# Kernel tuning notes

Measured on AMD Instinct MI355X. Metric: run time of the kernel, lower is better.

The kernel has to match this reference:

```python
import jax, jax.numpy as jnp
import numpy as np

FEATURE_DIM = 512
ACTION_DIM = 32
N_EXPERTS = 4
D_HIDDEN = 256
BATCH = 131072


def setup_inputs() -> dict:
    key = jax.random.key(0)
    ks = jax.random.split(key, 7)
    s_in = 1.0 / np.sqrt(FEATURE_DIM)
    s_h = 1.0 / np.sqrt(D_HIDDEN)
    return {
        "features": jax.random.normal(ks[0], (BATCH, FEATURE_DIM), dtype=jnp.float32),
        # gating network: feature_dim -> n_experts
        "Wg": jax.random.normal(ks[1], (FEATURE_DIM, N_EXPERTS), dtype=jnp.float32) * s_in,
        "bg": jnp.zeros((N_EXPERTS,), dtype=jnp.float32),
        # per-expert 2-layer MLP: feature_dim -> d_hidden -> action_dim
        "W1": jax.random.normal(ks[2], (N_EXPERTS, FEATURE_DIM, D_HIDDEN), dtype=jnp.float32) * s_in,
        "b1": jnp.zeros((N_EXPERTS, D_HIDDEN), dtype=jnp.float32),
        "W2": jax.random.normal(ks[3], (N_EXPERTS, D_HIDDEN, ACTION_DIM), dtype=jnp.float32) * s_h,
        "b2": jnp.zeros((N_EXPERTS, ACTION_DIM), dtype=jnp.float32),
    }


def reference(features, Wg, bg, W1, b1, W2, b2):
    # gate: softmax over experts, shape [b, e]
    gate = jax.nn.softmax(features @ Wg + bg, axis=-1)
    # expert MLPs (dense MoE: every expert sees every token)
    h = jax.nn.relu(jnp.einsum("bf,efh->beh", features, W1) + b1)  # [b, e, h]
    expert_out = jnp.einsum("beh,eha->bea", h, W2) + b2            # [b, e, a]
    # gate-weighted mixture -> action mean [b, a]
    action_mean = jnp.einsum("bea,be->ba", expert_out, gate)
    return action_mean
```

## Files before the change

kernel.cpp:

```cpp
#include <hip/hip_runtime.h>
#include <hip/hip_bf16.h>
#include <math.h>

#define FDIM 512
#define NEXP 4
#define HDIM 256
#define ADIM 32
#define BM   128
#define NTHR 512

typedef __attribute__((ext_vector_type(8))) short frag8;
typedef __attribute__((ext_vector_type(4))) float f32x4;

#define W1T_OFF 0
#define W2T_OFF (4*256*512)
#define WGT_OFF (W2T_OFF + 4*32*256)

__device__ inline ushort f2bf(float x) {
    union { float f; unsigned u; } v; v.f = x;
    unsigned r = v.u + 0x7FFFu + ((v.u >> 16) & 1u);
    return (ushort)(r >> 16);
}

__device__ inline frag8 pack8(f32x4 a, f32x4 b) {
    frag8 r;
    r[0] = (short)f2bf(a[0]); r[1] = (short)f2bf(a[1]);
    r[2] = (short)f2bf(a[2]); r[3] = (short)f2bf(a[3]);
    r[4] = (short)f2bf(b[0]); r[5] = (short)f2bf(b[1]);
    r[6] = (short)f2bf(b[2]); r[7] = (short)f2bf(b[3]);
    return r;
}

__device__ __forceinline__ void gl16(const void* g, void* l) {
    __builtin_amdgcn_global_load_lds(
        (const __attribute__((address_space(1))) unsigned int*)g,
        (__attribute__((address_space(3))) unsigned int*)l, 16, 0, 0);
}

__global__ __launch_bounds__(256) void moe_prep(const float* __restrict__ Wg,
                                                const float* __restrict__ W1,
                                                const float* __restrict__ W2,
                                                ushort* __restrict__ ws) {
    const int b = blockIdx.x, t = threadIdx.x;
    if (b < 64) {
        #pragma unroll
        for (int it = 0; it < 4; ++it) {
            int oct = (b * 256 + t) + it * 16384;
            int n = oct & 255, k8 = (oct >> 8) & 63, e = oct >> 14;
            f32x4 v0, v1;
            #pragma unroll
            for (int j = 0; j < 4; ++j) v0[j] = W1[(e*512 + k8*8 + j)*256 + n];
            #pragma unroll
            for (int j = 0; j < 4; ++j) v1[j] = W1[(e*512 + k8*8 + 4 + j)*256 + n];
            *(frag8*)(ws + W1T_OFF + (e*HDIM + n)*FDIM + k8*8) = pack8(v0, v1);
        }
    } else if (b < 80) {
        int oct = (b - 64) * 256 + t;
        int a = oct & 31, n8 = (oct >> 5) & 31, e = oct >> 10;
        f32x4 v0, v1;
        #pragma unroll
        for (int j = 0; j < 4; ++j) v0[j] = W2[(e*HDIM + n8*8 + j)*ADIM + a];
        #pragma unroll
        for (int j = 0; j < 4; ++j) v1[j] = W2[(e*HDIM + n8*8 + 4 + j)*ADIM + a];
        *(frag8*)(ws + W2T_OFF + (e*ADIM + a)*HDIM + n8*8) = pack8(v0, v1);
    } else {
        int oct = (b - 80) * 256 + t;
        int k8 = oct & 63, c = oct >> 6;
        f32x4 v0 = {0,0,0,0}, v1 = {0,0,0,0};
        if (c < NEXP) {
            #pragma unroll
            for (int j = 0; j < 4; ++j) v0[j] = Wg[(k8*8 + j)*NEXP + c];
            #pragma unroll
            for (int j = 0; j < 4; ++j) v1[j] = Wg[(k8*8 + 4 + j)*NEXP + c];
        }
        *(frag8*)(ws + WGT_OFF + c*FDIM + k8*8) = pack8(v0, v1);
    }
}

__global__ __launch_bounds__(NTHR, 2) void moe_main(
        const float* __restrict__ feat, const float* __restrict__ bg,
        const float* __restrict__ b1,  const float* __restrict__ b2,
        const ushort* __restrict__ ws, float* __restrict__ out) {
    __shared__ __attribute__((aligned(16))) unsigned char smem[65536 + 65536 + 16384 + 2048];
    unsigned char* bufA = smem;
    unsigned char* bufB = smem + 65536;
    unsigned char* wgtb = smem + 131072;
    float*         wgate = (float*)(smem + 147456);

    const int tid = threadIdx.x;
    const int lane = tid & 63;
    const int wave = tid >> 6;
    const int l15 = lane & 15;
    const int lg  = lane >> 4;
    const int row0 = blockIdx.x * BM;
    const int wrow = row0 + wave * 16;
    const ushort* w2t = ws + W2T_OFF;
    const char* w1b = (const char*)(ws + W1T_OFF);
    const char* wgb = (const char*)(ws + WGT_OFF);

    int sOff[8];
    #pragma unroll
    for (int j = 0; j < 8; ++j) {
        int slot = j * 512 + tid;
        int col  = slot >> 4;
        int kkp  = ((slot & 15) * 16) ^ ((col & 7) << 4);
        sOff[j]  = col * 1024 + kkp;
    }
    int gOff[2];
    #pragma unroll
    for (int j = 0; j < 2; ++j) {
        int slot = j * 512 + tid;
        int col  = slot >> 6;
        int off  = (slot & 63) * 16;
        gOff[j]  = col * 1024 + (off ^ ((col & 7) << 4));
    }

    #pragma unroll
    for (int j = 0; j < 2; ++j)
        gl16(wgb + gOff[j], wgtb + j * 8192 + wave * 1024);
    #pragma unroll
    for (int j = 0; j < 8; ++j)
        gl16(w1b + sOff[j], bufA + j * 8192 + wave * 1024);

    frag8 afrag[16];
    const float* fp = feat + (size_t)(wrow + l15) * FDIM + lg * 8;
    #pragma unroll
    for (int g4 = 0; g4 < 4; ++g4) {
        f32x4 t0[4], t1[4];
        #pragma unroll
        for (int s = 0; s < 4; ++s) {
            const float* p = fp + (g4 * 4 + s) * 32;
            t0[s] = *(const f32x4*)p;
            t1[s] = *(const f32x4*)(p + 4);
        }
        #pragma unroll
        for (int s = 0; s < 4; ++s) afrag[g4 * 4 + s] = pack8(t0[s], t1[s]);
    }

    __syncthreads();

    {
        f32x4 ga = {0.f, 0.f, 0.f, 0.f};
        #pragma unroll
        for (int s = 0; s < 16; ++s) {
            frag8 bb = *(const frag8*)(wgtb + l15 * 1024 + ((s * 64 + lg * 16) ^ ((l15 & 7) << 4)));
            ga = __builtin_amdgcn_mfma_f32_16x16x32_bf16(afrag[s], bb, ga, 0, 0, 0);
        }
        float bgv = bg[l15 & 3];
        #pragma unroll
        for (int r = 0; r < 4; ++r) {
            float v = ga[r] + bgv;
            float m = fmaxf(v, __shfl_xor(v, 1));
            m = fmaxf(m, __shfl_xor(m, 2));
            float eV = expf(v - m);
            float sV = eV + __shfl_xor(eV, 1);
            sV += __shfl_xor(sV, 2);
            float g = eV / sV;
            if (l15 < NEXP) wgate[wave * 64 + (lg * 4 + r) * 4 + l15] = g;
        }
    }

    f32x4 act[2];
    act[0] = (f32x4){0.f, 0.f, 0.f, 0.f};
    act[1] = (f32x4){0.f, 0.f, 0.f, 0.f};

    for (int e = 0; e < NEXP; ++e) {
        f32x4 acc1[16];
        #pragma unroll
        for (int ct = 0; ct < 16; ++ct) acc1[ct] = (f32x4){0.f, 0.f, 0.f, 0.f};

        const char* wbase = w1b + e * 262144;

        #pragma unroll
        for (int c = 0; c < 4; ++c) {
            if (c < 3) {
                unsigned char* dst = ((c + 1) & 1) ? bufB : bufA;
                #pragma unroll
                for (int j = 0; j < 8; ++j)
                    gl16(wbase + (c + 1) * 256 + sOff[j], dst + j * 8192 + wave * 1024);
            }
            __syncthreads();
            unsigned char* src = (c & 1) ? bufB : bufA;
            #pragma unroll
            for (int s = 0; s < 4; ++s) {
                #pragma unroll
                for (int ct = 0; ct < 16; ++ct) {
                    frag8 bb = *(const frag8*)(src + (ct * 16 + l15) * 256 +
                                               ((s * 64 + lg * 16) ^ ((l15 & 7) << 4)));
                    acc1[ct] = __builtin_amdgcn_mfma_f32_16x16x32_bf16(
                        afrag[c * 4 + s], bb, acc1[ct], 0, 0, 0);
                }
            }
            if (c < 3) __syncthreads();
        }

        unsigned char* hb = bufA + wave * 8192;
        #pragma unroll
        for (int ct = 0; ct < 16; ++ct) {
            float b1v = b1[e * HDIM + ct * 16 + l15];
            #pragma unroll
            for (int r = 0; r < 4; ++r) {
                int row = lg * 4 + r;
                float v = fmaxf(acc1[ct][r] + b1v, 0.f);
                *(ushort*)(hb + row * 512 + (((ct * 16 + l15) * 2) ^ ((row & 7) << 4))) = f2bf(v);
            }
        }
        asm volatile("s_waitcnt lgkmcnt(0)" ::: "memory");
        __builtin_amdgcn_sched_barrier(0);

        f32x4 acc2[2];
        acc2[0] = (f32x4){0.f, 0.f, 0.f, 0.f};
        acc2[1] = (f32x4){0.f, 0.f, 0.f, 0.f};
        #pragma unroll
        for (int s2 = 0; s2 < 8; ++s2) {
            frag8 ha = *(const frag8*)(hb + l15 * 512 + ((s2 * 64 + lg * 16) ^ ((l15 & 7) << 4)));
            #pragma unroll
            for (int ct2 = 0; ct2 < 2; ++ct2) {
                frag8 bb = *(const frag8*)(w2t + (e * ADIM + ct2 * 16 + l15) * HDIM + (s2 * 4 + lg) * 8);
                acc2[ct2] = __builtin_amdgcn_mfma_f32_16x16x32_bf16(ha, bb, acc2[ct2], 0, 0, 0);
            }
        }
        #pragma unroll
        for (int ct2 = 0; ct2 < 2; ++ct2) {
            float b2v = b2[e * ADIM + ct2 * 16 + l15];
            #pragma unroll
            for (int r = 0; r < 4; ++r) {
                float g = wgate[wave * 64 + (lg * 4 + r) * 4 + e];
                act[ct2][r] += g * (acc2[ct2][r] + b2v);
            }
        }

        if (e < 3) {
            __syncthreads();
            const char* nb = w1b + (e + 1) * 262144;
            #pragma unroll
            for (int j = 0; j < 8; ++j)
                gl16(nb + sOff[j], bufA + j * 8192 + wave * 1024);
        }
    }

    #pragma unroll
    for (int ct2 = 0; ct2 < 2; ++ct2)
        #pragma unroll
        for (int r = 0; r < 4; ++r)
            out[(size_t)(wrow + lg * 4 + r) * ADIM + ct2 * 16 + l15] = act[ct2][r];
}

extern "C" void kernel_launch(void* const* d_in, const int* in_sizes, int n_in,
                              void* d_out, int out_size, void* d_ws, size_t ws_size,
                              hipStream_t stream) {
    const float* feat = (const float*)d_in[0];
    const float* Wg   = (const float*)d_in[1];
    const float* bg   = (const float*)d_in[2];
    const float* W1   = (const float*)d_in[3];
    const float* b1   = (const float*)d_in[4];
    const float* W2   = (const float*)d_in[5];
    const float* b2   = (const float*)d_in[6];
    float* out = (float*)d_out;
    ushort* ws = (ushort*)d_ws;

    moe_prep<<<84, 256, 0, stream>>>(Wg, W1, W2, ws);
    const int nblk = 131072 / BM;
    moe_main<<<nblk, NTHR, 0, stream>>>(feat, bg, b1, b2, ws, out);
}
```

Before: 694.6 us.

## Split hidden dim into halves with continuous double-buffered W1 pipeline across experts

Each expert's layer-1 GEMM is split into two 128-column halves, and the 32KB W1 chunks are streamed through a ping-pong buffer as one continuous 32-step pipeline across experts and halves. This removes the per-expert pipeline drain and reload stall. W2 is now staged into LDS instead of being read from global memory inside the layer-2 loop, and the hidden activations get a dedicated LDS region. The change halves the acc1 register footprint, which frees VGPRs, but it adds a barrier on every chunk and depends on the buffer-ordering logic across iterations being correct.

```diff
diff --git a/kernel.cpp b/kernel.cpp
--- a/kernel.cpp
+++ b/kernel.cpp
@@ -81,10 +81,11 @@
         const float* __restrict__ feat, const float* __restrict__ bg,
         const float* __restrict__ b1,  const float* __restrict__ b2,
         const ushort* __restrict__ ws, float* __restrict__ out) {
-    __shared__ __attribute__((aligned(16))) unsigned char smem[65536 + 65536 + 16384 + 2048];
-    unsigned char* bufA = smem;
-    unsigned char* bufB = smem + 65536;
-    unsigned char* wgtb = smem + 131072;
+    __shared__ __attribute__((aligned(16))) unsigned char smem[149504];
+    unsigned char* buf0 = smem;
+    unsigned char* buf1 = smem + 32768;
+    unsigned char* w2b  = smem + 65536;
+    unsigned char* hbuf = smem + 81920;
     float*         wgate = (float*)(smem + 147456);
 
     const int tid = threadIdx.x;
@@ -94,47 +95,44 @@
     const int lg  = lane >> 4;
     const int row0 = blockIdx.x * BM;
     const int wrow = row0 + wave * 16;
-    const ushort* w2t = ws + W2T_OFF;
     const char* w1b = (const char*)(ws + W1T_OFF);
+    const char* w2g = (const char*)(ws + W2T_OFF);
     const char* wgb = (const char*)(ws + WGT_OFF);
 
-    int sOff[8];
-    #pragma unroll
-    for (int j = 0; j < 8; ++j) {
-        int slot = j * 512 + tid;
-        int col  = slot >> 4;
-        int kkp  = ((slot & 15) * 16) ^ ((col & 7) << 4);
-        sOff[j]  = col * 1024 + kkp;
-    }
-    int gOff[2];
+    int thrOff[4], w2Off[2], gOff[2];
+    #pragma unroll
+    for (int j = 0; j < 4; ++j) {
+        int slot = j * 512 + tid, cl = slot >> 4;
+        thrOff[j] = cl * 1024 + (((slot & 15) * 16) ^ ((cl & 7) << 4));
+    }
     #pragma unroll
     for (int j = 0; j < 2; ++j) {
-        int slot = j * 512 + tid;
-        int col  = slot >> 6;
-        int off  = (slot & 63) * 16;
-        gOff[j]  = col * 1024 + (off ^ ((col & 7) << 4));
-    }
-
-    #pragma unroll
-    for (int j = 0; j < 2; ++j)
-        gl16(wgb + gOff[j], wgtb + j * 8192 + wave * 1024);
-    #pragma unroll
-    for (int j = 0; j < 8; ++j)
-        gl16(w1b + sOff[j], bufA + j * 8192 + wave * 1024);
+        int slot = j * 512 + tid, c2 = slot >> 5;
+        w2Off[j] = c2 * 512 + (((slot & 31) * 16) ^ ((c2 & 7) << 4));
+        int cg = slot >> 6;
+        gOff[j] = cg * 1024 + (((slot & 63) * 16) ^ ((cg & 7) << 4));
+    }
+
+    #pragma unroll
+    for (int j = 0; j < 2; ++j) gl16(wgb + gOff[j], buf1 + j * 8192 + wave * 1024);
+    #pragma unroll
+    for (int j = 0; j < 4; ++j) gl16(w1b + thrOff[j], buf0 + j * 8192 + wave * 1024);
 
     frag8 afrag[16];
-    const float* fp = feat + (size_t)(wrow + l15) * FDIM + lg * 8;
-    #pragma unroll
-    for (int g4 = 0; g4 < 4; ++g4) {
-        f32x4 t0[4], t1[4];
-        #pragma unroll
-        for (int s = 0; s < 4; ++s) {
-            const float* p = fp + (g4 * 4 + s) * 32;
-            t0[s] = *(const f32x4*)p;
-            t1[s] = *(const f32x4*)(p + 4);
-        }
-        #pragma unroll
-        for (int s = 0; s < 4; ++s) afrag[g4 * 4 + s] = pack8(t0[s], t1[s]);
+    {
+        const float* fp = feat + (size_t)(wrow + l15) * FDIM + lg * 8;
+        #pragma unroll
+        for (int g4 = 0; g4 < 4; ++g4) {
+            f32x4 t0[4], t1[4];
+            #pragma unroll
+            for (int s = 0; s < 4; ++s) {
+                const float* p = fp + (g4 * 4 + s) * 32;
+                t0[s] = *(const f32x4*)p;
+                t1[s] = *(const f32x4*)(p + 4);
+            }
+            #pragma unroll
+            for (int s = 0; s < 4; ++s) afrag[g4 * 4 + s] = pack8(t0[s], t1[s]);
+        }
     }
 
     __syncthreads();
@@ -143,7 +141,7 @@
         f32x4 ga = {0.f, 0.f, 0.f, 0.f};
         #pragma unroll
         for (int s = 0; s < 16; ++s) {
-            frag8 bb = *(const frag8*)(wgtb + l15 * 1024 + ((s * 64 + lg * 16) ^ ((l15 & 7) << 4)));
+            frag8 bb = *(const frag8*)(buf1 + l15 * 1024 + ((s * 64 + lg * 16) ^ ((l15 & 7) << 4)));
             ga = __builtin_amdgcn_mfma_f32_16x16x32_bf16(afrag[s], bb, ga, 0, 0, 0);
         }
         float bgv = bg[l15 & 3];
@@ -155,87 +153,94 @@
             float eV = expf(v - m);
             float sV = eV + __shfl_xor(eV, 1);
             sV += __shfl_xor(sV, 2);
-            float g = eV / sV;
-            if (l15 < NEXP) wgate[wave * 64 + (lg * 4 + r) * 4 + l15] = g;
-        }
-    }
+            if (l15 < NEXP) wgate[wave * 64 + (lg * 4 + r) * 4 + l15] = eV / sV;
+        }
+    }
+    __syncthreads();
 
     f32x4 act[2];
     act[0] = (f32x4){0.f, 0.f, 0.f, 0.f};
     act[1] = (f32x4){0.f, 0.f, 0.f, 0.f};
 
     for (int e = 0; e < NEXP; ++e) {
-        f32x4 acc1[16];
-        #pragma unroll
-        for (int ct = 0; ct < 16; ++ct) acc1[ct] = (f32x4){0.f, 0.f, 0.f, 0.f};
-
-        const char* wbase = w1b + e * 262144;
-
-        #pragma unroll
-        for (int c = 0; c < 4; ++c) {
-            if (c < 3) {
-                unsigned char* dst = ((c + 1) & 1) ? bufB : bufA;
-                #pragma unroll
-                for (int j = 0; j < 8; ++j)
-                    gl16(wbase + (c + 1) * 256 + sOff[j], dst + j * 8192 + wave * 1024);
-            }
-            __syncthreads();
-            unsigned char* src = (c & 1) ? bufB : bufA;
-            #pragma unroll
-            for (int s = 0; s < 4; ++s) {
-                #pragma unroll
-                for (int ct = 0; ct < 16; ++ct) {
-                    frag8 bb = *(const frag8*)(src + (ct * 16 + l15) * 256 +
-                                               ((s * 64 + lg * 16) ^ ((l15 & 7) << 4)));
-                    acc1[ct] = __builtin_amdgcn_mfma_f32_16x16x32_bf16(
-                        afrag[c * 4 + s], bb, acc1[ct], 0, 0, 0);
-                }
-            }
-            if (c < 3) __syncthreads();
-        }
-
-        unsigned char* hb = bufA + wave * 8192;
-        #pragma unroll
-        for (int ct = 0; ct < 16; ++ct) {
-            float b1v = b1[e * HDIM + ct * 16 + l15];
-            #pragma unroll
-            for (int r = 0; r < 4; ++r) {
-                int row = lg * 4 + r;
-                float v = fmaxf(acc1[ct][r] + b1v, 0.f);
-                *(ushort*)(hb + row * 512 + (((ct * 16 + l15) * 2) ^ ((row & 7) << 4))) = f2bf(v);
-            }
-        }
+        #pragma unroll
+        for (int h = 0; h < 2; ++h) {
+            f32x4 acc1[8];
+            #pragma unroll
+            for (int ct = 0; ct < 8; ++ct) acc1[ct] = (f32x4){0.f, 0.f, 0.f, 0.f};
+
+            #pragma unroll
+            for (int c = 0; c < 4; ++c) {
+                const int g = e * 8 + h * 4 + c;
+                if (g < 31) {
+                    const int gn = g + 1;
+                    const char* sb = w1b + (gn >> 2) * 131072 + (gn & 3) * 256;
+                    unsigned char* db = (c & 1) ? buf0 : buf1;
+                    #pragma unroll
+                    for (int j = 0; j < 4; ++j)
+                        gl16(sb + thrOff[j], db + j * 8192 + wave * 1024);
+                }
+                if (h == 0 && c == 1) {
+                    const char* sb2 = w2g + e * 16384;
+                    #pragma unroll
+                    for (int j = 0; j < 2; ++j)
+                        gl16(sb2 + w2Off[j], w2b + j * 8192 + wave * 1024);
+                }
+                const unsigned char* src = (c & 1) ? buf1 : buf0;
+                #pragma unroll
+                for (int s = 0; s < 4; ++s) {
+                    #pragma unroll
+                    for (int ct = 0; ct < 8; ++ct) {
+                        frag8 bb = *(const frag8*)(src + (ct * 16 + l15) * 256 +
+                                                   ((s * 64 + lg * 16) ^ ((l15 & 7) << 4)));
+                        acc1[ct] = __builtin_amdgcn_mfma_f32_16x16x32_bf16(
+                            afrag[c * 4 + s], bb, acc1[ct], 0, 0, 0);
+                    }
+                }
+                __syncthreads();
+            }
+
+            unsigned char* hb = hbuf + wave * 8192;
+            #pragma unroll
+            for (int ct = 0; ct < 8; ++ct) {
+                int col = h * 128 + ct * 16 + l15;
+                float b1v = b1[e * HDIM + col];
+                #pragma unroll
+                for (int r = 0; r < 4; ++r) {
+                    int row = lg * 4 + r;
+                    float v = fmaxf(acc1[ct][r] + b1v, 0.f);
+                    *(ushort*)(hb + row * 512 + ((col * 2) ^ ((row & 7) << 4))) = f2bf(v);
+                }
+            }
+        }
+
         asm volatile("s_waitcnt lgkmcnt(0)" ::: "memory");
         __builtin_amdgcn_sched_barrier(0);
 
-        f32x4 acc2[2];
-        acc2[0] = (f32x4){0.f, 0.f, 0.f, 0.f};
-        acc2[1] = (f32x4){0.f, 0.f, 0.f, 0.f};
-        #pragma unroll
-        for (int s2 = 0; s2 < 8; ++s2) {
-            frag8 ha = *(const frag8*)(hb + l15 * 512 + ((s2 * 64 + lg * 16) ^ ((l15 & 7) << 4)));
+        {
+            f32x4 acc2[2];
+            acc2[0] = (f32x4){0.f, 0.f, 0.f, 0.f};
+            acc2[1] = (f32x4){0.f, 0.f, 0.f, 0.f};
+            const unsigned char* hb = hbuf + wave * 8192;
+            #pragma unroll
+            for (int s2 = 0; s2 < 8; ++s2) {
+                frag8 ha = *(const frag8*)(hb + l15 * 512 + ((s2 * 64 + lg * 16) ^ ((l15 & 7) << 4)));
+                #pragma unroll
+                for (int ct2 = 0; ct2 < 2; ++ct2) {
+                    frag8 bb = *(const frag8*)(w2b + (ct2 * 16 + l15) * 512 +
+                                               ((s2 * 64 + lg * 16) ^ ((l15 & 7) << 4)));
+                    acc2[ct2] = __builtin_amdgcn_mfma_f32_16x16x32_bf16(ha, bb, acc2[ct2], 0, 0, 0);
+                }
+            }
             #pragma unroll
             for (int ct2 = 0; ct2 < 2; ++ct2) {
-                frag8 bb = *(const frag8*)(w2t + (e * ADIM + ct2 * 16 + l15) * HDIM + (s2 * 4 + lg) * 8);
-                acc2[ct2] = __builtin_amdgcn_mfma_f32_16x16x32_bf16(ha, bb, acc2[ct2], 0, 0, 0);
-            }
-        }
-        #pragma unroll
-        for (int ct2 = 0; ct2 < 2; ++ct2) {
-            float b2v = b2[e * ADIM + ct2 * 16 + l15];
-            #pragma unroll
-            for (int r = 0; r < 4; ++r) {
-                float g = wgate[wave * 64 + (lg * 4 + r) * 4 + e];
-                act[ct2][r] += g * (acc2[ct2][r] + b2v);
-            }
-        }
-
-        if (e < 3) {
-            __syncthreads();
-            const char* nb = w1b + (e + 1) * 262144;
-            #pragma unroll
-            for (int j = 0; j < 8; ++j)
-                gl16(nb + sOff[j], bufA + j * 8192 + wave * 1024);
+                float b2v = b2[e * ADIM + ct2 * 16 + l15];
+                #pragma unroll
+                for (int r = 0; r < 4; ++r) {
+                    float gt = wgate[wave * 64 + (lg * 4 + r) * 4 + e];
+                    act[ct2][r] += gt * (acc2[ct2][r] + b2v);
+                }
+            }
         }
     }
 
```

New measurement: 575.0 us. 1.21x faster.
